# Kernel optimization log

Measured on AMD Instinct MI355X. Metric: run time of the kernel, lower is better.

Reference implementation:

```python
import jax, jax.numpy as jnp
import numpy as np

G, S, D, H = 32, 512, 128, 8   # num_groups, group_size, embed_dim, num_heads
HD = D // H                     # head_dim = 16
FFN = 2 * D                     # GLU hidden dim (ffn_dim = embed_dim * 2)
EPS = 1e-6


def _rmsnorm(x, w):
    return x * jax.lax.rsqrt(jnp.mean(x * x, axis=-1, keepdims=True) + EPS) * w


def setup_inputs() -> dict:
    key = jax.random.key(0)
    ks = jax.random.split(key, 12)
    BM = G * S
    s = 1.0 / float(np.sqrt(D))
    w = lambda k, shp, sc: (jax.random.normal(k, shp, jnp.float32) * sc)
    return {
        "x": jax.random.normal(ks[0], (BM, D), jnp.float32),
        "pe": jax.random.normal(ks[1], (BM, D), jnp.float32),
        "coords": jax.random.randint(ks[2], (BM, 4), 0, 128, jnp.int32),
        "Wq": w(ks[3], (D, D), s), "Wk": w(ks[4], (D, D), s),
        "Wv": w(ks[5], (D, D), s), "Wg": w(ks[6], (D, D), s),
        "Wo": w(ks[7], (D, D), s),
        "ln1_w": jnp.ones((D,), jnp.float32),
        "ln2_w": jnp.ones((D,), jnp.float32),
        "W_fc1": w(ks[8], (D, FFN), s),
        "W_gate": w(ks[9], (D, FFN), s),
        "W_fc2": w(ks[10], (FFN, D), 1.0 / float(np.sqrt(FFN))),
    }


def _decay_mask(coords):
    # coords: (BM,4) int; cols 1..3 are x,y,z voxel indices
    c = coords.reshape(G, S, 4)[..., 1:4].astype(jnp.float32)          # (G,S,3)
    dist = jnp.abs(c[:, :, None, :] - c[:, None, :, :]).sum(-1)        # (G,S,S) Manhattan
    decay = jnp.log(1.0 - 2.0 ** (-5.0 - jnp.arange(H, dtype=jnp.float32)))  # (H,)
    m = jnp.exp(dist[None] * decay[:, None, None, None])               # (H,G,S,S)
    m = jnp.nan_to_num(m)
    m = m / jnp.sqrt(m.sum(-1, keepdims=True))
    return jnp.transpose(m, (1, 0, 2, 3))                              # (G,H,S,S)


def reference(x, pe, coords, Wq, Wk, Wv, Wg, Wo, ln1_w, ln2_w, W_fc1, W_gate, W_fc2):
    mask = _decay_mask(coords)                                         # (G,H,S,S)

    # --- retention block (pre-norm) ---
    residual = x
    xn = _rmsnorm(x, ln1_w).reshape(G, S, D)
    qin = xn + pe.reshape(G, S, D)

    heads = lambda t: t.reshape(G, S, H, HD).transpose(0, 2, 1, 3)     # (G,H,S,HD)
    q = heads(qin @ Wq) * (HD ** -0.5)
    k = heads(qin @ Wk)
    v = heads(xn @ Wv)
    g = xn @ Wg                                                        # (G,S,D)

    qk = jnp.einsum('ghsd,ghtd->ghst', q, k)                           # (G,H,S,S)
    attn = jax.nn.softmax(qk, axis=-1) * mask
    denom = jnp.clip(jax.lax.stop_gradient(jnp.abs(attn).sum(-1, keepdims=True)), 1.0, None)
    attn = attn / denom
    o = jnp.einsum('ghst,ghtd->ghsd', attn, v)                         # (G,H,S,HD)
    # per-head RMSNorm (no affine), as group_norm over head_dim
    o = o * jax.lax.rsqrt(jnp.mean(o * o, axis=-1, keepdims=True) + EPS)
    o = o.transpose(0, 2, 1, 3).reshape(G, S, D)
    o = jax.nn.silu(g) * o                                             # swish output gate
    o = (o @ Wo).reshape(G * S, D)
    x1 = residual + o

    # --- GLU FFN block (pre-norm) ---
    h = _rmsnorm(x1, ln2_w)
    h = jax.nn.gelu(h @ W_fc1) * (h @ W_gate)
    return x1 + h @ W_fc2
```

## Files before the change

kernel.cpp:

```cpp
#include <hip/hip_runtime.h>

#define G_ 32
#define S_ 512
#define D_ 128
#define H_ 8
#define BM_ (G_*S_)
#define EPSF 1e-6f
#define VP_ 516

typedef float f32x4  __attribute__((ext_vector_type(4)));
typedef float f32x16 __attribute__((ext_vector_type(16)));
typedef short s16x8  __attribute__((ext_vector_type(8)));

typedef unsigned int uint32;

#if __has_builtin(__builtin_amdgcn_exp2f)
#define EXP2F(x) __builtin_amdgcn_exp2f(x)
#else
#define EXP2F(x) exp2f(x)
#endif

static __device__ __forceinline__ unsigned short f2bf(float f){
  uint32 u = __float_as_uint(f);
  u = (u + 0x7fffu + ((u >> 16) & 1u)) >> 16;
  return (unsigned short)u;
}
static __device__ __forceinline__ float bf2f(unsigned short h){
  return __uint_as_float(((uint32)h) << 16);
}
static __device__ __forceinline__ float siluf(float x){
  float e = EXP2F(-x * 1.4426950408889634f);
  return x / (1.0f + e);
}
static __device__ __forceinline__ float geluf(float x){
  float y = 0.7978845608028654f * (x + 0.044715f * x * x * x);
  y = fminf(fmaxf(y, -40.0f), 40.0f);
  float e = EXP2F(y * 2.8853900817779268f);
  float th = (e - 1.0f) / (e + 1.0f);
  return 0.5f * x * (1.0f + th);
}
static __device__ __forceinline__ uint32 sad3(uint32 a, uint32 b){
#if __has_builtin(__builtin_amdgcn_sad_u8)
  return __builtin_amdgcn_sad_u8(a, b, 0u);
#else
  uint32 d; uint32 z = 0;
  asm("v_sad_u8 %0, %1, %2, %3" : "=v"(d) : "v"(a), "v"(b), "v"(z));
  return d;
#endif
}

__global__ __launch_bounds__(256) void k_wprep_all(
    const float* __restrict__ w0, const float* __restrict__ w1,
    const float* __restrict__ w2, const float* __restrict__ w3,
    const float* __restrict__ w4, const float* __restrict__ w5,
    const float* __restrict__ w6, const float* __restrict__ w7,
    unsigned short* __restrict__ o0, unsigned short* __restrict__ o1,
    unsigned short* __restrict__ o2, unsigned short* __restrict__ o3,
    unsigned short* __restrict__ o4, unsigned short* __restrict__ o5,
    unsigned short* __restrict__ o6, unsigned short* __restrict__ o7){
  const int id = blockIdx.x * 256 + threadIdx.x;
  const float* W; unsigned short* O; int Kd, Nd, lid;
  if (id < 81920){
    const int which = id >> 14;
    W = (which == 0) ? w0 : (which == 1) ? w1 : (which == 2) ? w2 : (which == 3) ? w3 : w4;
    O = (which == 0) ? o0 : (which == 1) ? o1 : (which == 2) ? o2 : (which == 3) ? o3 : o4;
    Kd = 128; Nd = 128; lid = id & 16383;
  } else if (id < 114688){ W = w5; O = o5; Kd = 128; Nd = 256; lid = id - 81920; }
  else if (id < 147456){   W = w6; O = o6; Kd = 128; Nd = 256; lid = id - 114688; }
  else if (id < 180224){   W = w7; O = o7; Kd = 256; Nd = 128; lid = id - 147456; }
  else return;
  const int n = lid / Kd, k = lid - n * Kd;
  O[lid] = f2bf(W[(size_t)k * Nd + n]);
}

__global__ __launch_bounds__(512) void k_qkvg(
    const float* __restrict__ x, const float* __restrict__ pe,
    const float* __restrict__ ln1,
    const unsigned short* __restrict__ wqt, const unsigned short* __restrict__ wkt,
    const unsigned short* __restrict__ wvt, const unsigned short* __restrict__ wgt,
    unsigned short* __restrict__ qbf, unsigned short* __restrict__ kbf,
    unsigned short* __restrict__ vbf, unsigned short* __restrict__ gbf){
  __shared__ unsigned short wt[128 * 136];
  const int which = blockIdx.y;
  const unsigned short* WT = (which == 0) ? wqt : (which == 1) ? wkt : (which == 2) ? wvt : wgt;
  unsigned short* out      = (which == 0) ? qbf : (which == 1) ? kbf : (which == 2) ? vbf : gbf;
  const float scale = (which == 0) ? 0.36067376022224085f : 1.0f;
  const int tid = threadIdx.x;
  #pragma unroll
  for (int c = 0; c < 4; ++c){
    const int id8 = c * 512 + tid;
    const int n = id8 >> 4, k8 = id8 & 15;
    *(uint4*)&wt[n * 136 + k8 * 8] = *(const uint4*)&WT[n * 128 + k8 * 8];
  }
  const int lane = tid & 63, wave = tid >> 6;
  const int lr = lane & 15, lh = lane >> 4;
  const int rowbase = blockIdx.x * 128 + wave * 16;
  const size_t xb = (size_t)(rowbase + lr) * 128 + lh * 8;
  float xv[32];
  float ss = 0.f;
  #pragma unroll
  for (int kc = 0; kc < 4; ++kc){
    const float4 a = *(const float4*)&x[xb + kc * 32];
    const float4 b = *(const float4*)&x[xb + kc * 32 + 4];
    xv[kc*8+0]=a.x; xv[kc*8+1]=a.y; xv[kc*8+2]=a.z; xv[kc*8+3]=a.w;
    xv[kc*8+4]=b.x; xv[kc*8+5]=b.y; xv[kc*8+6]=b.z; xv[kc*8+7]=b.w;
    ss += a.x*a.x + a.y*a.y + a.z*a.z + a.w*a.w;
    ss += b.x*b.x + b.y*b.y + b.z*b.z + b.w*b.w;
  }
  ss += __shfl_xor(ss, 16, 64);
  ss += __shfl_xor(ss, 32, 64);
  const float rs = rsqrtf(ss * (1.0f / 128.0f) + EPSF);
  s16x8 af[4];
  #pragma unroll
  for (int kc = 0; kc < 4; ++kc){
    const float4 w0 = *(const float4*)&ln1[kc * 32 + lh * 8];
    const float4 w1 = *(const float4*)&ln1[kc * 32 + lh * 8 + 4];
    float n0 = xv[kc*8+0]*rs*w0.x, n1 = xv[kc*8+1]*rs*w0.y;
    float n2 = xv[kc*8+2]*rs*w0.z, n3 = xv[kc*8+3]*rs*w0.w;
    float n4 = xv[kc*8+4]*rs*w1.x, n5 = xv[kc*8+5]*rs*w1.y;
    float n6 = xv[kc*8+6]*rs*w1.z, n7 = xv[kc*8+7]*rs*w1.w;
    if (which < 2){
      const float4 p0 = *(const float4*)&pe[xb + kc * 32];
      const float4 p1 = *(const float4*)&pe[xb + kc * 32 + 4];
      n0 += p0.x; n1 += p0.y; n2 += p0.z; n3 += p0.w;
      n4 += p1.x; n5 += p1.y; n6 += p1.z; n7 += p1.w;
    }
    s16x8 r;
    r[0]=(short)f2bf(n0); r[1]=(short)f2bf(n1); r[2]=(short)f2bf(n2); r[3]=(short)f2bf(n3);
    r[4]=(short)f2bf(n4); r[5]=(short)f2bf(n5); r[6]=(short)f2bf(n6); r[7]=(short)f2bf(n7);
    af[kc] = r;
  }
  __syncthreads();
  #pragma unroll
  for (int ct = 0; ct < 8; ++ct){
    f32x4 acc = (f32x4)(0.0f);
    #pragma unroll
    for (int kc = 0; kc < 4; ++kc)
      acc = __builtin_amdgcn_mfma_f32_16x16x32_bf16(af[kc],
              *(const s16x8*)&wt[(ct * 16 + lr) * 136 + kc * 32 + lh * 8], acc, 0, 0, 0);
    #pragma unroll
    for (int j = 0; j < 4; ++j){
      const int row = rowbase + lh * 4 + j;
      const int col = ct * 16 + lr;
      out[(size_t)row * 128 + col] = f2bf(acc[j] * scale);
    }
  }
}

__global__ __launch_bounds__(256, 4) void k_attn(const unsigned short* __restrict__ qb,
    const unsigned short* __restrict__ kb, const unsigned short* __restrict__ vb,
    const int* __restrict__ coords, unsigned short* __restrict__ ob){
  __shared__ unsigned short vlT[16 * VP_];
  __shared__ uint32 cl1[S_];
  const int bx = blockIdx.x;
  const int g = bx >> 5, head = (bx >> 2) & 7, qtile = bx & 3;
  const int tid = threadIdx.x;
  const size_t rb = (size_t)g * S_ * 128 + head * 16;
  const int lane = tid & 63, wave = tid >> 6;
  const int lq = lane & 31, half = lane >> 5;
  const int qrow = qtile * 128 + wave * 32 + lq;
  const s16x8 bq = *(const s16x8*)(qb + rb + (size_t)qrow * 128 + half * 8);
  #pragma unroll
  for (int r = tid; r < S_; r += 256){
    const int4 cc = ((const int4*)coords)[g * S_ + r];
    cl1[r] = (uint32)(cc.y & 127) | ((uint32)(cc.z & 127) << 8) | ((uint32)(cc.w & 127) << 16);
  }
  {
    const int r0 = tid * 2;
    const unsigned short* v0 = vb + rb + (size_t)r0 * 128;
    const uint4 a0 = ((const uint4*)v0)[0], a1 = ((const uint4*)v0)[1];
    const uint4 b0 = ((const uint4*)(v0 + 128))[0], b1 = ((const uint4*)(v0 + 128))[1];
    const unsigned short* pa0 = (const unsigned short*)&a0;
    const unsigned short* pa1 = (const unsigned short*)&a1;
    const unsigned short* pb0 = (const unsigned short*)&b0;
    const unsigned short* pb1 = (const unsigned short*)&b1;
    #pragma unroll
    for (int hd = 0; hd < 8; ++hd){
      *(uint32*)&vlT[hd * VP_ + r0] = (uint32)pa0[hd] | ((uint32)pb0[hd] << 16);
      *(uint32*)&vlT[(hd + 8) * VP_ + r0] = (uint32)pa1[hd] | ((uint32)pb1[hd] << 16);
    }
  }
  __syncthreads();
  const float decay2 = log2f(1.0f - EXP2F(-(float)(5 + head)));
  const uint32 cs = cl1[qrow];
  f32x16 accO = (f32x16)(0.0f);
  float2 zm0 = {0.f,0.f}, zm1 = {0.f,0.f}, zm2 = {0.f,0.f}, zm3 = {0.f,0.f};
  const int vrow = (lq & 15) * VP_;
  for (int tc = 0; tc < 16; ++tc){
    const s16x8 ak = *(const s16x8*)(kb + rb + (size_t)(tc * 32 + lq) * 128 + half * 8);
    const uint4 cq0 = *(const uint4*)&cl1[tc * 32 + 4 * half];
    const uint4 cq1 = *(const uint4*)&cl1[tc * 32 + 8 + 4 * half];
    const uint4 cq2 = *(const uint4*)&cl1[tc * 32 + 16 + 4 * half];
    const uint4 cq3 = *(const uint4*)&cl1[tc * 32 + 24 + 4 * half];
    const f32x16 c = __builtin_amdgcn_mfma_f32_32x32x16_bf16(ak, bq, (f32x16)(0.0f), 0, 0, 0);
    float wv[16];
    #pragma unroll
    for (int i = 0; i < 16; ++i){
      const uint4& cq = (i < 4) ? cq0 : (i < 8) ? cq1 : (i < 12) ? cq2 : cq3;
      const uint32 ct1 = (&cq.x)[i & 3];
      const uint32 dist = sad3(cs, ct1);
      const float e2 = EXP2F((float)dist * decay2);
      const float e1 = EXP2F(c[i]);
      wv[i] = e1 * e2;
      float2& zm = (i & 2) ? ((i & 1) ? zm3 : zm2) : ((i & 1) ? zm1 : zm0);
      zm.x += e1; zm.y += e2;
    }
    union { uint32 u[4]; s16x8 v; } f0, f1;
    #pragma unroll
    for (int j = 0; j < 4; ++j){
      asm("v_cvt_pk_bf16_f32 %0, %1, %2" : "=v"(f0.u[j]) : "v"(wv[2 * j]), "v"(wv[2 * j + 1]));
      asm("v_cvt_pk_bf16_f32 %0, %1, %2" : "=v"(f1.u[j]) : "v"(wv[8 + 2 * j]), "v"(wv[9 + 2 * j]));
    }
    const int vcol = tc * 32 + 4 * half;
    union { uint32 u[4]; s16x8 v; } bv0, bv1;
    *(uint2*)&bv0.u[0] = *(const uint2*)&vlT[vrow + vcol];
    *(uint2*)&bv0.u[2] = *(const uint2*)&vlT[vrow + vcol + 8];
    *(uint2*)&bv1.u[0] = *(const uint2*)&vlT[vrow + vcol + 16];
    *(uint2*)&bv1.u[2] = *(const uint2*)&vlT[vrow + vcol + 24];
    accO = __builtin_amdgcn_mfma_f32_32x32x16_bf16(f0.v, bv0.v, accO, 0, 0, 0);
    accO = __builtin_amdgcn_mfma_f32_32x32x16_bf16(f1.v, bv1.v, accO, 0, 0, 0);
  }
  float Z = (zm0.x + zm1.x) + (zm2.x + zm3.x);
  float M = (zm0.y + zm1.y) + (zm2.y + zm3.y);
  Z += __shfl_xor(Z, 32, 64);
  M += __shfl_xor(M, 32, 64);
  const float sc = Z * sqrtf(M);
  const float epsp = EPSF * sc * sc;
  const size_t qbase = (size_t)(g * S_ + qtile * 128 + wave * 32);
  const int sub = (lq >> 4);
  #pragma unroll
  for (int ii = 0; ii < 8; ++ii){
    const int i = sub * 8 + ii;
    const int r = (i & 3) + 8 * (i >> 2) + 4 * half;
    const float v = accO[i];
    float ss = v * v;
    ss += __shfl_xor(ss, 1, 64); ss += __shfl_xor(ss, 2, 64);
    ss += __shfl_xor(ss, 4, 64); ss += __shfl_xor(ss, 8, 64);
    const float ei = __shfl(epsp, r, 64);
    const float on = v * rsqrtf(ss * 0.0625f + ei);
    ob[(qbase + r) * 128 + head * 16 + (lq & 15)] = f2bf(on);
  }
}

__global__ __launch_bounds__(256) void k_wo(const unsigned short* __restrict__ g,
    const unsigned short* __restrict__ o, const unsigned short* __restrict__ WT,
    const float* __restrict__ resid, float* __restrict__ outp){
  __shared__ unsigned short wt[64 * 136];
  const int y = blockIdx.y;
  const int tid = threadIdx.x;
  #pragma unroll
  for (int c = 0; c < 4; ++c){
    const int id8 = c * 256 + tid;
    const int n = id8 >> 4, k8 = id8 & 15;
    *(uint4*)&wt[n * 136 + k8 * 8] = *(const uint4*)&WT[(size_t)(y * 64 + n) * 128 + k8 * 8];
  }
  const int lane = tid & 63, wave = tid >> 6;
  const int lr = lane & 15, lh = lane >> 4;
  const int rowbase = blockIdx.x * 64 + wave * 16;
  s16x8 af[4];
  const size_t abase = (size_t)(rowbase + lr) * 128 + lh * 8;
  #pragma unroll
  for (int kc = 0; kc < 4; ++kc){
    const s16x8 gv = *(const s16x8*)(g + abase + kc * 32);
    const s16x8 ov = *(const s16x8*)(o + abase + kc * 32);
    s16x8 r;
    #pragma unroll
    for (int j = 0; j < 8; ++j)
      r[j] = (short)f2bf(siluf(bf2f((unsigned short)gv[j])) * bf2f((unsigned short)ov[j]));
    af[kc] = r;
  }
  __syncthreads();
  #pragma unroll
  for (int ct = 0; ct < 4; ++ct){
    f32x4 acc = (f32x4)(0.0f);
    #pragma unroll
    for (int kc = 0; kc < 4; ++kc)
      acc = __builtin_amdgcn_mfma_f32_16x16x32_bf16(af[kc],
              *(const s16x8*)&wt[(ct * 16 + lr) * 136 + kc * 32 + lh * 8], acc, 0, 0, 0);
    #pragma unroll
    for (int j = 0; j < 4; ++j){
      const int row = rowbase + lh * 4 + j;
      const int col = y * 64 + ct * 16 + lr;
      const size_t idx = (size_t)row * 128 + col;
      outp[idx] = acc[j] + resid[idx];
    }
  }
}

__global__ __launch_bounds__(256) void k_dual(const float* __restrict__ x1,
    const float* __restrict__ ln2,
    const unsigned short* __restrict__ W1T, const unsigned short* __restrict__ W2T,
    unsigned short* __restrict__ hh){
  __shared__ unsigned short w1l[128 * 136];
  __shared__ unsigned short w2l[128 * 136];
  const int y = blockIdx.y;
  const int tid = threadIdx.x;
  #pragma unroll
  for (int c = 0; c < 8; ++c){
    const int id8 = c * 256 + tid;
    const int n = id8 >> 4, k8 = id8 & 15;
    *(uint4*)&w1l[n * 136 + k8 * 8] = *(const uint4*)&W1T[(size_t)(y * 128 + n) * 128 + k8 * 8];
    *(uint4*)&w2l[n * 136 + k8 * 8] = *(const uint4*)&W2T[(size_t)(y * 128 + n) * 128 + k8 * 8];
  }
  const int lane = tid & 63, wave = tid >> 6;
  const int lr = lane & 15, lh = lane >> 4;
  const int rowbase = blockIdx.x * 64 + wave * 16;
  const size_t xb = (size_t)(rowbase + lr) * 128 + lh * 8;
  float xv[32];
  float ss = 0.f;
  #pragma unroll
  for (int kc = 0; kc < 4; ++kc){
    const float4 a = *(const float4*)&x1[xb + kc * 32];
    const float4 b = *(const float4*)&x1[xb + kc * 32 + 4];
    xv[kc*8+0]=a.x; xv[kc*8+1]=a.y; xv[kc*8+2]=a.z; xv[kc*8+3]=a.w;
    xv[kc*8+4]=b.x; xv[kc*8+5]=b.y; xv[kc*8+6]=b.z; xv[kc*8+7]=b.w;
    ss += a.x*a.x + a.y*a.y + a.z*a.z + a.w*a.w;
    ss += b.x*b.x + b.y*b.y + b.z*b.z + b.w*b.w;
  }
  ss += __shfl_xor(ss, 16, 64);
  ss += __shfl_xor(ss, 32, 64);
  const float rs = rsqrtf(ss * (1.0f / 128.0f) + EPSF);
  s16x8 af[4];
  #pragma unroll
  for (int kc = 0; kc < 4; ++kc){
    const float4 w0 = *(const float4*)&ln2[kc * 32 + lh * 8];
    const float4 w1 = *(const float4*)&ln2[kc * 32 + lh * 8 + 4];
    s16x8 r;
    r[0]=(short)f2bf(xv[kc*8+0]*rs*w0.x); r[1]=(short)f2bf(xv[kc*8+1]*rs*w0.y);
    r[2]=(short)f2bf(xv[kc*8+2]*rs*w0.z); r[3]=(short)f2bf(xv[kc*8+3]*rs*w0.w);
    r[4]=(short)f2bf(xv[kc*8+4]*rs*w1.x); r[5]=(short)f2bf(xv[kc*8+5]*rs*w1.y);
    r[6]=(short)f2bf(xv[kc*8+6]*rs*w1.z); r[7]=(short)f2bf(xv[kc*8+7]*rs*w1.w);
    af[kc] = r;
  }
  __syncthreads();
  #pragma unroll
  for (int ct = 0; ct < 8; ++ct){
    f32x4 a1 = (f32x4)(0.0f), a2 = (f32x4)(0.0f);
    #pragma unroll
    for (int kc = 0; kc < 4; ++kc){
      a1 = __builtin_amdgcn_mfma_f32_16x16x32_bf16(af[kc],
             *(const s16x8*)&w1l[(ct * 16 + lr) * 136 + kc * 32 + lh * 8], a1, 0, 0, 0);
      a2 = __builtin_amdgcn_mfma_f32_16x16x32_bf16(af[kc],
             *(const s16x8*)&w2l[(ct * 16 + lr) * 136 + kc * 32 + lh * 8], a2, 0, 0, 0);
    }
    #pragma unroll
    for (int j = 0; j < 4; ++j){
      const int row = rowbase + lh * 4 + j;
      const int col = y * 128 + ct * 16 + lr;
      hh[(size_t)row * 256 + col] = f2bf(geluf(a1[j]) * a2[j]);
    }
  }
}

__global__ __launch_bounds__(256) void k_fc2(const unsigned short* __restrict__ hh,
    const unsigned short* __restrict__ WT, const float* __restrict__ x1,
    float* __restrict__ outp){
  __shared__ unsigned short wt[64 * 264];
  const int y = blockIdx.y;
  const int tid = threadIdx.x;
  #pragma unroll
  for (int c = 0; c < 8; ++c){
    const int id8 = c * 256 + tid;
    const int n = id8 >> 5, k8 = id8 & 31;
    *(uint4*)&wt[n * 264 + k8 * 8] = *(const uint4*)&WT[(size_t)(y * 64 + n) * 256 + k8 * 8];
  }
  const int lane = tid & 63, wave = tid >> 6;
  const int lr = lane & 15, lh = lane >> 4;
  const int rowbase = blockIdx.x * 64 + wave * 16;
  s16x8 af[8];
  const unsigned short* arow = hh + (size_t)(rowbase + lr) * 256 + lh * 8;
  #pragma unroll
  for (int kc = 0; kc < 8; ++kc) af[kc] = *(const s16x8*)(arow + kc * 32);
  __syncthreads();
  #pragma unroll
  for (int ct = 0; ct < 4; ++ct){
    f32x4 acc = (f32x4)(0.0f);
    #pragma unroll
    for (int kc = 0; kc < 8; ++kc)
      acc = __builtin_amdgcn_mfma_f32_16x16x32_bf16(af[kc],
              *(const s16x8*)&wt[(ct * 16 + lr) * 264 + kc * 32 + lh * 8], acc, 0, 0, 0);
    #pragma unroll
    for (int j = 0; j < 4; ++j){
      const int row = rowbase + lh * 4 + j;
      const int col = y * 64 + ct * 16 + lr;
      const size_t idx = (size_t)row * 128 + col;
      outp[idx] = acc[j] + x1[idx];
    }
  }
}

extern "C" void kernel_launch(void* const* d_in, const int* in_sizes, int n_in,
                              void* d_out, int out_size, void* d_ws, size_t ws_size,
                              hipStream_t stream){
  const float* x     = (const float*)d_in[0];
  const float* pe    = (const float*)d_in[1];
  const int*   coords= (const int*)d_in[2];
  const float* Wq    = (const float*)d_in[3];
  const float* Wk    = (const float*)d_in[4];
  const float* Wv    = (const float*)d_in[5];
  const float* Wg    = (const float*)d_in[6];
  const float* Wo    = (const float*)d_in[7];
  const float* ln1   = (const float*)d_in[8];
  const float* ln2   = (const float*)d_in[9];
  const float* Wfc1  = (const float*)d_in[10];
  const float* Wgate = (const float*)d_in[11];
  const float* Wfc2  = (const float*)d_in[12];
  float* out = (float*)d_out;
  char* ws = (char*)d_ws;

  const size_t SZB = 4194304;
  unsigned short* qbf  = (unsigned short*)(ws);
  unsigned short* kbf  = (unsigned short*)(ws + 1 * SZB);
  unsigned short* vbf  = (unsigned short*)(ws + 2 * SZB);
  unsigned short* gbf  = (unsigned short*)(ws + 3 * SZB);
  unsigned short* obf  = (unsigned short*)(ws + 4 * SZB);
  float*          x1   = (float*)(ws + 5 * SZB);
  unsigned short* hhb  = (unsigned short*)(ws + 5 * SZB + 8388608);
  char* wbase = ws + 5 * SZB + 2 * 8388608;
  unsigned short* wqt   = (unsigned short*)(wbase);
  unsigned short* wkt   = (unsigned short*)(wbase + 32768);
  unsigned short* wvt   = (unsigned short*)(wbase + 65536);
  unsigned short* wgt   = (unsigned short*)(wbase + 98304);
  unsigned short* wot   = (unsigned short*)(wbase + 131072);
  unsigned short* fc1t  = (unsigned short*)(wbase + 163840);
  unsigned short* gatet = (unsigned short*)(wbase + 229376);
  unsigned short* fc2t  = (unsigned short*)(wbase + 294912);

  dim3 b256(256);
  k_wprep_all<<<704, b256, 0, stream>>>(Wq, Wk, Wv, Wg, Wo, Wfc1, Wgate, Wfc2,
                                        wqt, wkt, wvt, wgt, wot, fc1t, gatet, fc2t);
  k_qkvg<<<dim3(128, 4), dim3(512), 0, stream>>>(x, pe, ln1, wqt, wkt, wvt, wgt,
                                                 qbf, kbf, vbf, gbf);
  k_attn<<<1024, b256, 0, stream>>>(qbf, kbf, vbf, coords, obf);
  k_wo<<<dim3(256, 2), b256, 0, stream>>>(gbf, obf, wot, x, x1);
  k_dual<<<dim3(256, 2), b256, 0, stream>>>(x1, ln2, fc1t, gatet, hhb);
  k_fc2<<<dim3(256, 2), b256, 0, stream>>>(hhb, fc2t, x1, out);
}
```

Measured before the change: 82.18 us.

## Split attention key loop across two wave groups with LDS reduction

The attention kernel now runs 512 threads per block. Two groups of four waves each process half of the key tiles for the same query rows. The upper group writes its partial output accumulators and Z/M sums into reused shared memory, and the lower group adds them in before normalizing. This doubles the wave count per block to hide latency in the serial key loop, at the cost of extra syncs, an LDS round trip, and tighter register limits from launch_bounds(512, 8).

Result: slower. 111.4 us (+35.5%).

```diff
diff --git a/kernel.cpp b/kernel.cpp
--- a/kernel.cpp
+++ b/kernel.cpp
@@ -147,7 +147,7 @@
   }
 }
 
-__global__ __launch_bounds__(256, 4) void k_attn(const unsigned short* __restrict__ qb,
+__global__ __launch_bounds__(512, 8) void k_attn(const unsigned short* __restrict__ qb,
     const unsigned short* __restrict__ kb, const unsigned short* __restrict__ vb,
     const int* __restrict__ coords, unsigned short* __restrict__ ob){
   __shared__ unsigned short vlT[16 * VP_];
@@ -157,15 +157,11 @@
   const int tid = threadIdx.x;
   const size_t rb = (size_t)g * S_ * 128 + head * 16;
   const int lane = tid & 63, wave = tid >> 6;
+  const int qsub = wave & 3, thalf = wave >> 2;
   const int lq = lane & 31, half = lane >> 5;
-  const int qrow = qtile * 128 + wave * 32 + lq;
+  const int qrow = qtile * 128 + qsub * 32 + lq;
   const s16x8 bq = *(const s16x8*)(qb + rb + (size_t)qrow * 128 + half * 8);
-  #pragma unroll
-  for (int r = tid; r < S_; r += 256){
-    const int4 cc = ((const int4*)coords)[g * S_ + r];
-    cl1[r] = (uint32)(cc.y & 127) | ((uint32)(cc.z & 127) << 8) | ((uint32)(cc.w & 127) << 16);
-  }
-  {
+  if (tid < 256){
     const int r0 = tid * 2;
     const unsigned short* v0 = vb + rb + (size_t)r0 * 128;
     const uint4 a0 = ((const uint4*)v0)[0], a1 = ((const uint4*)v0)[1];
@@ -179,6 +175,12 @@
       *(uint32*)&vlT[hd * VP_ + r0] = (uint32)pa0[hd] | ((uint32)pb0[hd] << 16);
       *(uint32*)&vlT[(hd + 8) * VP_ + r0] = (uint32)pa1[hd] | ((uint32)pb1[hd] << 16);
     }
+  } else {
+    const int t2 = (tid - 256) * 2;
+    const int4 c0 = ((const int4*)coords)[g * S_ + t2];
+    const int4 c1 = ((const int4*)coords)[g * S_ + t2 + 1];
+    cl1[t2]     = (uint32)(c0.y & 127) | ((uint32)(c0.z & 127) << 8) | ((uint32)(c0.w & 127) << 16);
+    cl1[t2 + 1] = (uint32)(c1.y & 127) | ((uint32)(c1.z & 127) << 8) | ((uint32)(c1.w & 127) << 16);
   }
   __syncthreads();
   const float decay2 = log2f(1.0f - EXP2F(-(float)(5 + head)));
@@ -186,7 +188,8 @@
   f32x16 accO = (f32x16)(0.0f);
   float2 zm0 = {0.f,0.f}, zm1 = {0.f,0.f}, zm2 = {0.f,0.f}, zm3 = {0.f,0.f};
   const int vrow = (lq & 15) * VP_;
-  for (int tc = 0; tc < 16; ++tc){
+  for (int tci = 0; tci < 8; ++tci){
+    const int tc = thalf * 8 + tci;
     const s16x8 ak = *(const s16x8*)(kb + rb + (size_t)(tc * 32 + lq) * 128 + half * 8);
     const uint4 cq0 = *(const uint4*)&cl1[tc * 32 + 4 * half];
     const uint4 cq1 = *(const uint4*)&cl1[tc * 32 + 8 + 4 * half];
@@ -224,21 +227,42 @@
   float M = (zm0.y + zm1.y) + (zm2.y + zm3.y);
   Z += __shfl_xor(Z, 32, 64);
   M += __shfl_xor(M, 32, 64);
-  const float sc = Z * sqrtf(M);
-  const float epsp = EPSF * sc * sc;
-  const size_t qbase = (size_t)(g * S_ + qtile * 128 + wave * 32);
-  const int sub = (lq >> 4);
-  #pragma unroll
-  for (int ii = 0; ii < 8; ++ii){
-    const int i = sub * 8 + ii;
-    const int r = (i & 3) + 8 * (i >> 2) + 4 * half;
-    const float v = accO[i];
-    float ss = v * v;
-    ss += __shfl_xor(ss, 1, 64); ss += __shfl_xor(ss, 2, 64);
-    ss += __shfl_xor(ss, 4, 64); ss += __shfl_xor(ss, 8, 64);
-    const float ei = __shfl(epsp, r, 64);
-    const float on = v * rsqrtf(ss * 0.0625f + ei);
-    ob[(qbase + r) * 128 + head * 16 + (lq & 15)] = f2bf(on);
+  __syncthreads();
+  {
+    float* dumpO  = (float*)vlT;
+    float* dumpZM = (float*)cl1;
+    if (wave >= 4){
+      const int p = wave & 3;
+      #pragma unroll
+      for (int i = 0; i < 16; ++i) dumpO[p * 1024 + i * 64 + lane] = accO[i];
+      dumpZM[p * 128 + lane]      = Z;
+      dumpZM[p * 128 + 64 + lane] = M;
+    }
+  }
+  __syncthreads();
+  if (wave < 4){
+    const float* dumpO  = (const float*)vlT;
+    const float* dumpZM = (const float*)cl1;
+    #pragma unroll
+    for (int i = 0; i < 16; ++i) accO[i] += dumpO[wave * 1024 + i * 64 + lane];
+    Z += dumpZM[wave * 128 + lane];
+    M += dumpZM[wave * 128 + 64 + lane];
+    const float sc = Z * sqrtf(M);
+    const float epsp = EPSF * sc * sc;
+    const size_t qbase = (size_t)(g * S_ + qtile * 128 + qsub * 32);
+    const int sub = (lq >> 4);
+    #pragma unroll
+    for (int ii = 0; ii < 8; ++ii){
+      const int i = sub * 8 + ii;
+      const int r = (i & 3) + 8 * (i >> 2) + 4 * half;
+      const float v = accO[i];
+      float ss = v * v;
+      ss += __shfl_xor(ss, 1, 64); ss += __shfl_xor(ss, 2, 64);
+      ss += __shfl_xor(ss, 4, 64); ss += __shfl_xor(ss, 8, 64);
+      const float ei = __shfl(epsp, r, 64);
+      const float on = v * rsqrtf(ss * 0.0625f + ei);
+      ob[(qbase + r) * 128 + head * 16 + (lq & 15)] = f2bf(on);
+    }
   }
 }
 
@@ -431,7 +455,7 @@
                                         wqt, wkt, wvt, wgt, wot, fc1t, gatet, fc2t);
   k_qkvg<<<dim3(128, 4), dim3(512), 0, stream>>>(x, pe, ln1, wqt, wkt, wvt, wgt,
                                                  qbf, kbf, vbf, gbf);
-  k_attn<<<1024, b256, 0, stream>>>(qbf, kbf, vbf, coords, obf);
+  k_attn<<<1024, dim3(512), 0, stream>>>(qbf, kbf, vbf, coords, obf);
   k_wo<<<dim3(256, 2), b256, 0, stream>>>(gbf, obf, wot, x, x1);
   k_dual<<<dim3(256, 2), b256, 0, stream>>>(x1, ln2, fc1t, gatet, hhb);
   k_fc2<<<dim3(256, 2), b256, 0, stream>>>(hhb, fc2t, x1, out);
```
